# Kernel tuning notes

Hardware: AMD Instinct MI355X
Metric: run time of the kernel (lower is better)

Reference implementation:

```python
import jax, jax.numpy as jnp
import numpy as np

D = 1024
H = 16
HD = D // H
B = 2
S = 2048


def setup_inputs() -> dict:
    key = jax.random.key(0)
    ks = jax.random.split(key, 9)
    sc = 1.0 / np.sqrt(D)
    return {
        "x": jax.random.normal(ks[0], (B, S, D), dtype=jnp.float32),
        "attention_mask": jnp.ones((B, S), dtype=jnp.int32),
        "Wq": jax.random.normal(ks[1], (D, D), dtype=jnp.float32) * sc,
        "bq": jax.random.normal(ks[2], (D,), dtype=jnp.float32) * 0.02,
        "Wk": jax.random.normal(ks[3], (D, D), dtype=jnp.float32) * sc,
        "bk": jax.random.normal(ks[4], (D,), dtype=jnp.float32) * 0.02,
        "Wv": jax.random.normal(ks[5], (D, D), dtype=jnp.float32) * sc,
        "bv": jax.random.normal(ks[6], (D,), dtype=jnp.float32) * 0.02,
        "Wo": jax.random.normal(ks[7], (D, D), dtype=jnp.float32) * sc,
        "bo": jax.random.normal(ks[8], (D,), dtype=jnp.float32) * 0.02,
    }


def reference(x, attention_mask, Wq, bq, Wk, bk, Wv, bv, Wo, bo):
    Bb, Ss, d = x.shape
    # projections (torch Linear: x @ W.T + b; here W stored as [in,out])
    q = (x @ Wq + bq).reshape(Bb, Ss, H, HD).transpose(0, 2, 1, 3)  # [B,H,S,hd]
    k = (x @ Wk + bk).reshape(Bb, Ss, H, HD).transpose(0, 2, 1, 3)
    v = (x @ Wv + bv).reshape(Bb, Ss, H, HD).transpose(0, 2, 1, 3)
    dots = jnp.einsum("bhqd,bhkd->bhqk", q, k) / np.sqrt(HD)  # [B,H,S,S]
    causal = jnp.triu(jnp.ones((Ss, Ss), dtype=bool), k=1)  # True above diagonal
    dots = jnp.where(causal[None, None], -jnp.inf, dots)
    pad = (attention_mask == 0)[:, None, None, :]  # [B,1,1,S]
    dots = jnp.where(pad, -jnp.inf, dots)
    scores = jax.nn.softmax(dots, axis=-1)
    o = jnp.einsum("bhqk,bhkd->bhqd", scores, v)  # [B,H,S,hd]
    o = o.transpose(0, 2, 1, 3).reshape(Bb, Ss, d)
    return o @ Wo + bo
```

## Files before the change

### kernel.cpp

```cpp
#include <hip/hip_runtime.h>

#define D_  1024
#define H_  16
#define HD_ 64
#define B_  2
#define S_  2048
#define M_  (B_*S_)

typedef _Float16 f16;
typedef _Float16 f16x8 __attribute__((ext_vector_type(8)));
typedef _Float16 f16x4 __attribute__((ext_vector_type(4)));
typedef _Float16 f16x2 __attribute__((ext_vector_type(2)));
typedef __fp16   h16x2 __attribute__((ext_vector_type(2)));
typedef float    f32x4 __attribute__((ext_vector_type(4)));

#define GLOAD_LDS16(g, l) \
  __builtin_amdgcn_global_load_lds((__attribute__((address_space(1))) const void*)(g), \
                                   (__attribute__((address_space(3))) void*)(l), 16, 0, 0)

__global__ void k_cvt_x(const float* __restrict__ x, f16* __restrict__ xb) {
  int i = blockIdx.x * blockDim.x + threadIdx.x;
  float4 v = ((const float4*)x)[i];
  f16x4 o = { (f16)v.x, (f16)v.y, (f16)v.z, (f16)v.w };
  ((f16x4*)xb)[i] = o;
}

__global__ void k_twt4(const float* __restrict__ Wq, const float* __restrict__ Wk,
                       const float* __restrict__ Wv, const float* __restrict__ Wo,
                       f16* __restrict__ WT) {
  __shared__ float t[32][33];
  int z = blockIdx.z;
  const float* W = (z == 0) ? Wq : (z == 1) ? Wk : (z == 2) ? Wv : Wo;
  f16* out = WT + (size_t)z * D_ * D_;
  int n0 = blockIdx.x * 32, k0 = blockIdx.y * 32;
  int tx = threadIdx.x, ty = threadIdx.y;
  #pragma unroll
  for (int i = 0; i < 4; i++)
    t[ty + i*8][tx] = W[(size_t)(k0 + ty + i*8) * D_ + n0 + tx];
  __syncthreads();
  #pragma unroll
  for (int i = 0; i < 4; i++)
    out[(size_t)(n0 + ty + i*8) * D_ + k0 + tx] = (f16)t[tx][ty + i*8];
}

template<int MODE>
__device__ __forceinline__ void gemm_body(const f16* __restrict__ A,
                                          const f16* __restrict__ Bt,
                                          const float* __restrict__ bias,
                                          void* __restrict__ Cout) {
  __shared__ __align__(16) f16 lA[2][128 * 32];
  __shared__ __align__(16) f16 lB[2][128 * 32];
  const int tid = threadIdx.x;
  const int wv = tid >> 6, lane = tid & 63;
  const int m0 = blockIdx.y * 128, n0 = blockIdx.x * 128;
  const int fr = lane & 15, fg = lane >> 4;
  const int wm = wv >> 1, wn = wv & 1;
  const int srow = (lane >> 2), skk = (lane & 3) * 8;
  f32x4 acc[4][4] = {};

#define G_STAGE(k0_, c_) do { \
    _Pragma("unroll") \
    for (int it_ = 0; it_ < 2; ++it_) { \
      int ch_ = wv + it_ * 4; \
      int row_ = ch_ * 16 + srow; \
      GLOAD_LDS16(A  + (size_t)(m0 + row_) * D_ + (k0_) + skk, &lA[c_][ch_ * 512]); \
      GLOAD_LDS16(Bt + (size_t)(n0 + row_) * D_ + (k0_) + skk, &lB[c_][ch_ * 512]); \
    } \
  } while (0)

  G_STAGE(0, 0);
  __syncthreads();

  int c = 0;
  for (int k0 = 0; k0 < D_; k0 += 32) {
    if (k0 + 32 < D_) G_STAGE(k0 + 32, c ^ 1);
    f16x8 a[4], b[4];
    #pragma unroll
    for (int i = 0; i < 4; i++) a[i] = *(const f16x8*)&lA[c][(wm*64 + i*16 + fr) * 32 + fg * 8];
    #pragma unroll
    for (int j = 0; j < 4; j++) b[j] = *(const f16x8*)&lB[c][(wn*64 + j*16 + fr) * 32 + fg * 8];
    #pragma unroll
    for (int i = 0; i < 4; i++)
      #pragma unroll
      for (int j = 0; j < 4; j++)
        acc[i][j] = __builtin_amdgcn_mfma_f32_16x16x32_f16(a[i], b[j], acc[i][j], 0, 0, 0);
    __syncthreads();
    c ^= 1;
  }
#undef G_STAGE

  #pragma unroll
  for (int i = 0; i < 4; i++) {
    #pragma unroll
    for (int j = 0; j < 4; j++) {
      int grow0 = m0 + wm*64 + i*16 + fg*4;
      int gcol  = n0 + wn*64 + j*16 + fr;
      float bb = bias[gcol & (D_ - 1)];
      #pragma unroll
      for (int r = 0; r < 4; r++) {
        float val = acc[i][j][r] + bb;
        int grow = grow0 + r;
        if (MODE == 0) {
          int z = gcol >> 10, gl = gcol & (D_ - 1);
          int b = grow >> 11, s = grow & (S_ - 1);
          int h = gl >> 6,  hd = gl & (HD_ - 1);
          ((f16*)Cout)[(size_t)z * (M_ * D_) +
                       ((size_t)(b * H_ + h) * S_ + s) * HD_ + hd] = (f16)val;
        } else {
          ((float*)Cout)[(size_t)grow * D_ + gcol] = val;
        }
      }
    }
  }
}

__global__ __launch_bounds__(256) void k_gemm_qkv(const f16* __restrict__ A,
                                                  const f16* __restrict__ WT0,
                                                  const float* __restrict__ bq,
                                                  const float* __restrict__ bk,
                                                  const float* __restrict__ bv,
                                                  f16* __restrict__ qkv) {
  const int n0 = blockIdx.x * 128;
  const float* bias = (n0 < 1024) ? bq : (n0 < 2048) ? bk : bv;
  gemm_body<0>(A, WT0, bias, qkv);
}

__global__ __launch_bounds__(256) void k_gemm_out(const f16* __restrict__ A,
                                                  const f16* __restrict__ Bt,
                                                  const float* __restrict__ bias,
                                                  float* __restrict__ Cout) {
  gemm_body<1>(A, Bt, bias, Cout);
}

#define POFF 8.65617025f

__global__ __launch_bounds__(256) void k_attn(const f16* __restrict__ Qh,
                                              const f16* __restrict__ Kh,
                                              const f16* __restrict__ Vh,
                                              const int* __restrict__ am,
                                              f16* __restrict__ OpA, f16* __restrict__ OpB,
                                              float* __restrict__ lpA, float* __restrict__ lpB) {
  __shared__ __align__(16) f16 kt[2][64 * 64];
  __shared__ __align__(16) f16 vt[2][64 * 64];
  __shared__ __align__(16) f16 pl[4][32 * 64];

  const int tid = threadIdx.x;
  const int wv = tid >> 6, lane = tid & 63;
  const int fr = lane & 15, fg = lane >> 4;

  const int d = blockIdx.x;
  const int bh = d & 31;
  const int m  = (d >> 5) & 7;
  const int typeB = d >> 8;
  const int b = bh >> 4;

  f16*   Op = typeB ? OpB : OpA;
  float* lp = typeB ? lpB : lpA;

  const f16* Qb = Qh + (size_t)bh * S_ * HD_;
  const f16* Kb = Kh + (size_t)bh * S_ * HD_;
  const f16* Vb = Vh + (size_t)bh * S_ * HD_;
  const int* amb = am + b * S_;
  f16* plw = pl[wv];

  volatile int* flag = (volatile int*)&pl[0][0];
  if (tid == 0) *flag = 1;
  __syncthreads();
  {
    int mv = 1;
    #pragma unroll
    for (int i = 0; i < 8; ++i) mv &= amb[tid * 8 + i];
    if (!mv) *flag = 0;
  }
  __syncthreads();
  const bool allv = (*flag != 0);

  const f16 qs = (f16)0.18033688f;
  const int ksrc = 8 * ((lane & 7) ^ (lane >> 3));
  const int swz = (fr & 7) << 3;
  const int vkk = (tid >> 3) * 2, vd0 = (tid & 7) * 8;
  const int vswz2 = (tid & 3) << 4;
  const f32x4 cinit = { -POFF, -POFF, -POFF, -POFF };
  const f16 one_ = (f16)1.0f;
  const f16x8 onesf = { one_, one_, one_, one_, one_, one_, one_, one_ };

#define STAGE_K(t_, c_) do { \
    const f16* kp_ = Kb + (size_t)((t_) * 64) * HD_; \
    GLOAD_LDS16(kp_ + (size_t)((wv*2+0)*8 + (lane >> 3)) * HD_ + ksrc, &kt[c_][(wv*2+0)*512]); \
    GLOAD_LDS16(kp_ + (size_t)((wv*2+1)*8 + (lane >> 3)) * HD_ + ksrc, &kt[c_][(wv*2+1)*512]); \
  } while (0)

#define LOAD_V(t_) do { \
    const f16* vp_ = Vb + (size_t)((t_) * 64 + vkk) * HD_ + vd0; \
    vA = *(const f16x8*)vp_; vBr = *(const f16x8*)(vp_ + HD_); \
  } while (0)

#define WRITE_V(c_) do { \
    _Pragma("unroll") \
    for (int j_ = 0; j_ < 8; ++j_) { \
      f16x2 pr_ = { vA[j_], vBr[j_] }; \
      *(f16x2*)&vt[c_][(vd0 + j_) * 64 + ((vkk ^ (j_ << 3)) ^ vswz2)] = pr_; \
    } \
  } while (0)

  f16x8 vA, vBr;

  const int qts[2] = { m, 15 - m };
  int s_t0[2], s_t1[2];
  if (!typeB) {
    s_t0[0] = 0;     s_t1[0] = m + 1;
    s_t0[1] = 0;     s_t1[1] = 16 - m;
  } else {
    s_t0[0] = m + 1;  s_t1[0] = 2 * (m + 1);
    s_t0[1] = 16 - m; s_t1[1] = 2 * (16 - m);
  }

  STAGE_K(s_t0[0], 0);
  LOAD_V(s_t0[0]);
  WRITE_V(0);
  __syncthreads();

  int c = 0;
  for (int sg = 0; sg < 2; ++sg) {
    const int qt = qts[sg];
    const int q0w = qt * 128 + wv * 32;

    f16x8 qf[2][2];
    #pragma unroll
    for (int rt = 0; rt < 2; ++rt) {
      f16x8 r0 = *(const f16x8*)&Qb[(size_t)(q0w + rt*16 + fr) * HD_ + fg*8];
      f16x8 r1 = *(const f16x8*)&Qb[(size_t)(q0w + rt*16 + fr) * HD_ + 32 + fg*8];
      qf[rt][0] = r0 * qs; qf[rt][1] = r1 * qs;
    }

    f32x4 accO[2][4] = {};
    f32x4 accL[2] = {};

    for (int t = s_t0[sg]; t < s_t1[sg]; ++t) {
      int nt_ = -1;
      if (t + 1 < s_t1[sg]) nt_ = t + 1;
      else if (sg == 0)     nt_ = s_t0[1];
      if (nt_ >= 0) { STAGE_K(nt_, c ^ 1); LOAD_V(nt_); }

      const int kb = t * 64;
      const int dq = q0w - kb;
      if (dq + 31 >= 0) {
        int tm1 = (dq + 31) >> 4; if (tm1 > 3) tm1 = 3;
        int tm0 = (dq + 15) >> 4; if (tm0 > 3) tm0 = 3;
        const bool fullb = (dq >= 63);

        f32x4 s[2][4];
        #pragma unroll
        for (int rt = 0; rt < 2; ++rt)
          #pragma unroll
          for (int tt = 0; tt < 4; ++tt) s[rt][tt] = cinit;

        __builtin_amdgcn_s_setprio(1);
        #pragma unroll
        for (int tt = 0; tt < 4; ++tt) {
          if (tt <= tm1) {
            const int kr = (tt*16 + fr) * 64;
            f16x8 kf0 = *(const f16x8*)&kt[c][kr + ((     fg*8) ^ swz)];
            f16x8 kf1 = *(const f16x8*)&kt[c][kr + ((32 + fg*8) ^ swz)];
            s[1][tt] = __builtin_amdgcn_mfma_f32_16x16x32_f16(kf0, qf[1][0], s[1][tt], 0, 0, 0);
            s[1][tt] = __builtin_amdgcn_mfma_f32_16x16x32_f16(kf1, qf[1][1], s[1][tt], 0, 0, 0);
            if (tt <= tm0) {
              s[0][tt] = __builtin_amdgcn_mfma_f32_16x16x32_f16(kf0, qf[0][0], s[0][tt], 0, 0, 0);
              s[0][tt] = __builtin_amdgcn_mfma_f32_16x16x32_f16(kf1, qf[0][1], s[0][tt], 0, 0, 0);
            }
          }
        }
        __builtin_amdgcn_s_setprio(0);

        #pragma unroll
        for (int rt = 0; rt < 2; ++rt) {
          const int tmr = rt ? tm1 : tm0;
          if (tmr < 0) continue;
          const int thr = dq + rt*16 + fr;
          #pragma unroll
          for (int tt = 0; tt < 4; ++tt) {
            union { f16x4 v; h16x2 h[2]; } pk;
            pk.v = (f16x4){};
            if (tt <= tmr) {
              float p[4];
              if (allv) {
                #pragma unroll
                for (int r = 0; r < 4; ++r) {
                  float sv = s[rt][tt][r];
                  if (!fullb) sv = (tt*16 + fg*4 + r <= thr) ? sv : -1e30f;
                  p[r] = exp2f(sv);
                }
              } else {
                int4 a4 = *(const int4*)&amb[kb + tt*16 + fg*4];
                #pragma unroll
                for (int r = 0; r < 4; ++r) {
                  float sv = s[rt][tt][r];
                  if (!fullb) sv = (tt*16 + fg*4 + r <= thr) ? sv : -1e30f;
                  float pv = exp2f(sv);
                  int mr_ = (r == 0) ? a4.x : (r == 1) ? a4.y : (r == 2) ? a4.z : a4.w;
                  p[r] = mr_ ? pv : 0.0f;
                }
              }
              pk.h[0] = __builtin_amdgcn_cvt_pkrtz(p[0], p[1]);
              pk.h[1] = __builtin_amdgcn_cvt_pkrtz(p[2], p[3]);
            }
            *(f16x4*)&plw[(rt*16 + fr) * 64 + ((tt*16 + fg*4) ^ swz)] = pk.v;
          }
        }

        __builtin_amdgcn_s_setprio(1);
        #pragma unroll
        for (int ks = 0; ks < 2; ++ks) {
          if (ks <= (tm1 >> 1)) {
            f16x8 vf[4];
            #pragma unroll
            for (int nt = 0; nt < 4; ++nt)
              vf[nt] = *(const f16x8*)&vt[c][(nt*16 + fr) * 64 +
                           ((ks*32 + fg*8) ^ swz ^ (((2*nt + (fr >> 3)) & 3) << 4))];
            #pragma unroll
            for (int rt = 0; rt < 2; ++rt) {
              const int tmr = rt ? tm1 : tm0;
              if (tmr >= 0 && ks <= (tmr >> 1)) {
                f16x8 pa = *(const f16x8*)&plw[(rt*16 + fr) * 64 + ((ks*32 + fg*8) ^ swz)];
                #pragma unroll
                for (int nt = 0; nt < 4; ++nt)
                  accO[rt][nt] = __builtin_amdgcn_mfma_f32_16x16x32_f16(pa, vf[nt], accO[rt][nt], 0, 0, 0);
                accL[rt] = __builtin_amdgcn_mfma_f32_16x16x32_f16(pa, onesf, accL[rt], 0, 0, 0);
              }
            }
          }
        }
        __builtin_amdgcn_s_setprio(0);
      }

      if (nt_ >= 0) WRITE_V(c ^ 1);
      __syncthreads();
      c ^= 1;
    }

    #pragma unroll
    for (int rt = 0; rt < 2; ++rt) {
      if (fr == 0) {
        #pragma unroll
        for (int r = 0; r < 4; ++r)
          lp[(size_t)bh * S_ + q0w + rt*16 + fg*4 + r] = accL[rt][r];
      }
      f16* Oprow = Op + (size_t)bh * (S_ * HD_);
      #pragma unroll
      for (int nt = 0; nt < 4; ++nt) {
        int col = nt*16 + fr;
        #pragma unroll
        for (int r = 0; r < 4; ++r) {
          int row = q0w + rt*16 + fg*4 + r;
          Oprow[(size_t)row * HD_ + col] = (f16)accO[rt][nt][r];
        }
      }
    }
  }

#undef STAGE_K
#undef LOAD_V
#undef WRITE_V
}

__global__ __launch_bounds__(256) void k_comb(const f16* __restrict__ OA,
                                              const f16* __restrict__ OB,
                                              const float* __restrict__ lA,
                                              const float* __restrict__ lB,
                                              f16* __restrict__ Obf) {
  int gid = blockIdx.x * 256 + threadIdx.x;
  int seg = gid & 7, rowg = gid >> 3;
  int bh = rowg >> 11, row = rowg & 2047;
  f16x8 a  = ((const f16x8*)OA)[gid];
  f16x8 b2 = ((const f16x8*)OB)[gid];
  float inv = __builtin_amdgcn_rcpf(lA[rowg] + lB[rowg]);
  f16x8 o;
  #pragma unroll
  for (int j = 0; j < 8; ++j) o[j] = (f16)(((float)a[j] + (float)b2[j]) * inv);
  int bb = bh >> 4, hh = bh & 15;
  *(f16x8*)&Obf[((size_t)(bb * S_ + row)) * D_ + hh * 64 + seg * 8] = o;
}

extern "C" void kernel_launch(void* const* d_in, const int* in_sizes, int n_in,
                              void* d_out, int out_size, void* d_ws, size_t ws_size,
                              hipStream_t stream) {
  const float* x  = (const float*)d_in[0];
  const int*   am = (const int*)d_in[1];
  const float* Wq = (const float*)d_in[2];
  const float* bq = (const float*)d_in[3];
  const float* Wk = (const float*)d_in[4];
  const float* bk = (const float*)d_in[5];
  const float* Wv = (const float*)d_in[6];
  const float* bv = (const float*)d_in[7];
  const float* Wo = (const float*)d_in[8];
  const float* bo = (const float*)d_in[9];

  char* ws = (char*)d_ws;
  f16*   xb  = (f16*)(ws);
  f16*   wt  = (f16*)(ws + (8u  << 20));
  f16*   qkv = (f16*)(ws + (16u << 20));
  f16*   OpA = (f16*)(ws + (40u << 20));
  f16*   OpB = xb;
  float* lpA = (float*)(ws + (8u << 20));
  float* lpB = (float*)(ws + (8u << 20) + (256u << 10));
  f16*   Obf = qkv;

  k_cvt_x<<<4096, 256, 0, stream>>>(x, xb);

  dim3 tb(32, 8), tg4(32, 32, 4);
  k_twt4<<<tg4, tb, 0, stream>>>(Wq, Wk, Wv, Wo, wt);

  k_gemm_qkv<<<dim3(24, 32), 256, 0, stream>>>(xb, wt, bq, bk, bv, qkv);

  k_attn<<<dim3(512), 256, 0, stream>>>(qkv,
                                        qkv + (size_t)M_ * D_,
                                        qkv + 2 * (size_t)M_ * D_,
                                        am, OpA, OpB, lpA, lpB);

  k_comb<<<dim3(2048), 256, 0, stream>>>(OpA, OpB, lpA, lpB, Obf);

  k_gemm_out<<<dim3(8, 32), 256, 0, stream>>>(Obf, wt + 3 * (size_t)(D_ * D_), bo,
                                              (float*)d_out);
}
```

Baseline: 126.0 us.

## Triple-buffer K tiles and flatten attention loop into a two-ahead prefetch pipeline

Flattens the two query-tile segments into a single loop over all K/V tiles. K now uses a triple LDS buffer with async global-to-LDS staging issued two tiles ahead, and V register loads are likewise issued one iteration earlier. The block-wide sync is replaced by a barrier that waits only on older vector-memory ops (vmcnt(4)), so the next prefetch stays in flight across the barrier. This aims to hide global load latency behind MFMA work, at the cost of extra LDS, more register pressure, and hand-tuned waitcnt correctness risk.

```diff
diff --git a/kernel.cpp b/kernel.cpp
--- a/kernel.cpp
+++ b/kernel.cpp
@@ -134,13 +134,20 @@
 
 #define POFF 8.65617025f
 
+#define PIPE_BARRIER() do { \
+    asm volatile("s_waitcnt vmcnt(4) lgkmcnt(0)" ::: "memory"); \
+    __builtin_amdgcn_s_barrier(); \
+    asm volatile("" ::: "memory"); \
+    __builtin_amdgcn_sched_barrier(0); \
+  } while (0)
+
 __global__ __launch_bounds__(256) void k_attn(const f16* __restrict__ Qh,
                                               const f16* __restrict__ Kh,
                                               const f16* __restrict__ Vh,
                                               const int* __restrict__ am,
                                               f16* __restrict__ OpA, f16* __restrict__ OpB,
                                               float* __restrict__ lpA, float* __restrict__ lpB) {
-  __shared__ __align__(16) f16 kt[2][64 * 64];
+  __shared__ __align__(16) f16 kt[3][64 * 64];
   __shared__ __align__(16) f16 vt[2][64 * 64];
   __shared__ __align__(16) f16 pl[4][32 * 64];
 
@@ -206,144 +213,39 @@
   f16x8 vA, vBr;
 
   const int qts[2] = { m, 15 - m };
-  int s_t0[2], s_t1[2];
-  if (!typeB) {
-    s_t0[0] = 0;     s_t1[0] = m + 1;
-    s_t0[1] = 0;     s_t1[1] = 16 - m;
-  } else {
-    s_t0[0] = m + 1;  s_t1[0] = 2 * (m + 1);
-    s_t0[1] = 16 - m; s_t1[1] = 2 * (16 - m);
+  int t00, t01, t10, t11;
+  if (!typeB) { t00 = 0;      t01 = m + 1;        t10 = 0;      t11 = 16 - m; }
+  else        { t00 = m + 1;  t01 = 2 * (m + 1);  t10 = 16 - m; t11 = 2 * (16 - m); }
+  const int n0 = t01 - t00;
+  const int ntot = n0 + (t11 - t10);
+  #define TILE_OF(g_) (((g_) < n0) ? (t00 + (g_)) : (t10 + (g_) - n0))
+
+  LOAD_V(TILE_OF(0));
+  STAGE_K(TILE_OF(0), 0);
+  WRITE_V(0);
+  LOAD_V(TILE_OF(1));
+  STAGE_K(TILE_OF(1), 1);
+  PIPE_BARRIER();
+
+  int sg = 0;
+  int q0w = qts[0] * 128 + wv * 32;
+  f16x8 qf[2][2];
+  #pragma unroll
+  for (int rt = 0; rt < 2; ++rt) {
+    f16x8 r0 = *(const f16x8*)&Qb[(size_t)(q0w + rt*16 + fr) * HD_ + fg*8];
+    f16x8 r1 = *(const f16x8*)&Qb[(size_t)(q0w + rt*16 + fr) * HD_ + 32 + fg*8];
+    qf[rt][0] = r0 * qs; qf[rt][1] = r1 * qs;
   }
-
-  STAGE_K(s_t0[0], 0);
-  LOAD_V(s_t0[0]);
-  WRITE_V(0);
-  __syncthreads();
-
-  int c = 0;
-  for (int sg = 0; sg < 2; ++sg) {
-    const int qt = qts[sg];
-    const int q0w = qt * 128 + wv * 32;
-
-    f16x8 qf[2][2];
-    #pragma unroll
-    for (int rt = 0; rt < 2; ++rt) {
-      f16x8 r0 = *(const f16x8*)&Qb[(size_t)(q0w + rt*16 + fr) * HD_ + fg*8];
-      f16x8 r1 = *(const f16x8*)&Qb[(size_t)(q0w + rt*16 + fr) * HD_ + 32 + fg*8];
-      qf[rt][0] = r0 * qs; qf[rt][1] = r1 * qs;
-    }
-
-    f32x4 accO[2][4] = {};
-    f32x4 accL[2] = {};
-
-    for (int t = s_t0[sg]; t < s_t1[sg]; ++t) {
-      int nt_ = -1;
-      if (t + 1 < s_t1[sg]) nt_ = t + 1;
-      else if (sg == 0)     nt_ = s_t0[1];
-      if (nt_ >= 0) { STAGE_K(nt_, c ^ 1); LOAD_V(nt_); }
-
-      const int kb = t * 64;
-      const int dq = q0w - kb;
-      if (dq + 31 >= 0) {
-        int tm1 = (dq + 31) >> 4; if (tm1 > 3) tm1 = 3;
-        int tm0 = (dq + 15) >> 4; if (tm0 > 3) tm0 = 3;
-        const bool fullb = (dq >= 63);
-
-        f32x4 s[2][4];
-        #pragma unroll
-        for (int rt = 0; rt < 2; ++rt)
-          #pragma unroll
-          for (int tt = 0; tt < 4; ++tt) s[rt][tt] = cinit;
-
-        __builtin_amdgcn_s_setprio(1);
-        #pragma unroll
-        for (int tt = 0; tt < 4; ++tt) {
-          if (tt <= tm1) {
-            const int kr = (tt*16 + fr) * 64;
-            f16x8 kf0 = *(const f16x8*)&kt[c][kr + ((     fg*8) ^ swz)];
-            f16x8 kf1 = *(const f16x8*)&kt[c][kr + ((32 + fg*8) ^ swz)];
-            s[1][tt] = __builtin_amdgcn_mfma_f32_16x16x32_f16(kf0, qf[1][0], s[1][tt], 0, 0, 0);
-            s[1][tt] = __builtin_amdgcn_mfma_f32_16x16x32_f16(kf1, qf[1][1], s[1][tt], 0, 0, 0);
-            if (tt <= tm0) {
-              s[0][tt] = __builtin_amdgcn_mfma_f32_16x16x32_f16(kf0, qf[0][0], s[0][tt], 0, 0, 0);
-              s[0][tt] = __builtin_amdgcn_mfma_f32_16x16x32_f16(kf1, qf[0][1], s[0][tt], 0, 0, 0);
-            }
-          }
-        }
-        __builtin_amdgcn_s_setprio(0);
-
-        #pragma unroll
-        for (int rt = 0; rt < 2; ++rt) {
-          const int tmr = rt ? tm1 : tm0;
-          if (tmr < 0) continue;
-          const int thr = dq + rt*16 + fr;
-          #pragma unroll
-          for (int tt = 0; tt < 4; ++tt) {
-            union { f16x4 v; h16x2 h[2]; } pk;
-            pk.v = (f16x4){};
-            if (tt <= tmr) {
-              float p[4];
-              if (allv) {
-                #pragma unroll
-                for (int r = 0; r < 4; ++r) {
-                  float sv = s[rt][tt][r];
-                  if (!fullb) sv = (tt*16 + fg*4 + r <= thr) ? sv : -1e30f;
-                  p[r] = exp2f(sv);
-                }
-              } else {
-                int4 a4 = *(const int4*)&amb[kb + tt*16 + fg*4];
-                #pragma unroll
-                for (int r = 0; r < 4; ++r) {
-                  float sv = s[rt][tt][r];
-                  if (!fullb) sv = (tt*16 + fg*4 + r <= thr) ? sv : -1e30f;
-                  float pv = exp2f(sv);
-                  int mr_ = (r == 0) ? a4.x : (r == 1) ? a4.y : (r == 2) ? a4.z : a4.w;
-                  p[r] = mr_ ? pv : 0.0f;
-                }
-              }
-              pk.h[0] = __builtin_amdgcn_cvt_pkrtz(p[0], p[1]);
-              pk.h[1] = __builtin_amdgcn_cvt_pkrtz(p[2], p[3]);
-            }
-            *(f16x4*)&plw[(rt*16 + fr) * 64 + ((tt*16 + fg*4) ^ swz)] = pk.v;
-          }
-        }
-
-        __builtin_amdgcn_s_setprio(1);
-        #pragma unroll
-        for (int ks = 0; ks < 2; ++ks) {
-          if (ks <= (tm1 >> 1)) {
-            f16x8 vf[4];
-            #pragma unroll
-            for (int nt = 0; nt < 4; ++nt)
-              vf[nt] = *(const f16x8*)&vt[c][(nt*16 + fr) * 64 +
-                           ((ks*32 + fg*8) ^ swz ^ (((2*nt + (fr >> 3)) & 3) << 4))];
-            #pragma unroll
-            for (int rt = 0; rt < 2; ++rt) {
-              const int tmr = rt ? tm1 : tm0;
-              if (tmr >= 0 && ks <= (tmr >> 1)) {
-                f16x8 pa = *(const f16x8*)&plw[(rt*16 + fr) * 64 + ((ks*32 + fg*8) ^ swz)];
-                #pragma unroll
-                for (int nt = 0; nt < 4; ++nt)
-                  accO[rt][nt] = __builtin_amdgcn_mfma_f32_16x16x32_f16(pa, vf[nt], accO[rt][nt], 0, 0, 0);
-                accL[rt] = __builtin_amdgcn_mfma_f32_16x16x32_f16(pa, onesf, accL[rt], 0, 0, 0);
-              }
-            }
-          }
-        }
-        __builtin_amdgcn_s_setprio(0);
-      }
-
-      if (nt_ >= 0) WRITE_V(c ^ 1);
-      __syncthreads();
-      c ^= 1;
-    }
-
+  f32x4 accO[2][4] = {};
+  f32x4 accL[2] = {};
+
+  auto do_epi = [&](int q0w_) {
     #pragma unroll
     for (int rt = 0; rt < 2; ++rt) {
       if (fr == 0) {
         #pragma unroll
         for (int r = 0; r < 4; ++r)
-          lp[(size_t)bh * S_ + q0w + rt*16 + fg*4 + r] = accL[rt][r];
+          lp[(size_t)bh * S_ + q0w_ + rt*16 + fg*4 + r] = accL[rt][r];
       }
       f16* Oprow = Op + (size_t)bh * (S_ * HD_);
       #pragma unroll
@@ -351,13 +253,136 @@
         int col = nt*16 + fr;
         #pragma unroll
         for (int r = 0; r < 4; ++r) {
-          int row = q0w + rt*16 + fg*4 + r;
+          int row = q0w_ + rt*16 + fg*4 + r;
           Oprow[(size_t)row * HD_ + col] = (f16)accO[rt][nt][r];
         }
       }
     }
+  };
+
+  for (int g = 0; g < ntot; ++g) {
+    if (g == n0) {
+      do_epi(q0w);
+      sg = 1;
+      q0w = qts[1] * 128 + wv * 32;
+      #pragma unroll
+      for (int rt = 0; rt < 2; ++rt) {
+        f16x8 r0 = *(const f16x8*)&Qb[(size_t)(q0w + rt*16 + fr) * HD_ + fg*8];
+        f16x8 r1 = *(const f16x8*)&Qb[(size_t)(q0w + rt*16 + fr) * HD_ + 32 + fg*8];
+        qf[rt][0] = r0 * qs; qf[rt][1] = r1 * qs;
+        accL[rt] = (f32x4){};
+        #pragma unroll
+        for (int nt = 0; nt < 4; ++nt) accO[rt][nt] = (f32x4){};
+      }
+    }
+
+    const int t = TILE_OF(g);
+    const int cK = g % 3, cV = g & 1;
+
+    if (g + 1 < ntot) WRITE_V((g + 1) & 1);
+    if (g + 2 < ntot) {
+      const int tp = TILE_OF(g + 2);
+      LOAD_V(tp);
+      STAGE_K(tp, (g + 2) % 3);
+    }
+
+    const int kb = t * 64;
+    const int dq = q0w - kb;
+    if (dq + 31 >= 0) {
+      int tm1 = (dq + 31) >> 4; if (tm1 > 3) tm1 = 3;
+      int tm0 = (dq + 15) >> 4; if (tm0 > 3) tm0 = 3;
+      const bool fullb = (dq >= 63);
+
+      f32x4 s[2][4];
+      #pragma unroll
+      for (int rt = 0; rt < 2; ++rt)
+        #pragma unroll
+        for (int tt = 0; tt < 4; ++tt) s[rt][tt] = cinit;
+
+      __builtin_amdgcn_s_setprio(1);
+      #pragma unroll
+      for (int tt = 0; tt < 4; ++tt) {
+        if (tt <= tm1) {
+          const int kr = (tt*16 + fr) * 64;
+          f16x8 kf0 = *(const f16x8*)&kt[cK][kr + ((     fg*8) ^ swz)];
+          f16x8 kf1 = *(const f16x8*)&kt[cK][kr + ((32 + fg*8) ^ swz)];
+          s[1][tt] = __builtin_amdgcn_mfma_f32_16x16x32_f16(kf0, qf[1][0], s[1][tt], 0, 0, 0);
+          s[1][tt] = __builtin_amdgcn_mfma_f32_16x16x32_f16(kf1, qf[1][1], s[1][tt], 0, 0, 0);
+          if (tt <= tm0) {
+            s[0][tt] = __builtin_amdgcn_mfma_f32_16x16x32_f16(kf0, qf[0][0], s[0][tt], 0, 0, 0);
+            s[0][tt] = __builtin_amdgcn_mfma_f32_16x16x32_f16(kf1, qf[0][1], s[0][tt], 0, 0, 0);
+          }
+        }
+      }
+      __builtin_amdgcn_s_setprio(0);
+
+      #pragma unroll
+      for (int rt = 0; rt < 2; ++rt) {
+        const int tmr = rt ? tm1 : tm0;
+        if (tmr < 0) continue;
+        const int thr = dq + rt*16 + fr;
+        #pragma unroll
+        for (int tt = 0; tt < 4; ++tt) {
+          union { f16x4 v; h16x2 h[2]; } pk;
+          pk.v = (f16x4){};
+          if (tt <= tmr) {
+            float p[4];
+            if (allv) {
+              #pragma unroll
+              for (int r = 0; r < 4; ++r) {
+                float sv = s[rt][tt][r];
+                if (!fullb) sv = (tt*16 + fg*4 + r <= thr) ? sv : -1e30f;
+                p[r] = exp2f(sv);
+              }
+            } else {
+              int4 a4 = *(const int4*)&amb[kb + tt*16 + fg*4];
+              #pragma unroll
+              for (int r = 0; r < 4; ++r) {
+                float sv = s[rt][tt][r];
+                if (!fullb) sv = (tt*16 + fg*4 + r <= thr) ? sv : -1e30f;
+                float pv = exp2f(sv);
+                int mr_ = (r == 0) ? a4.x : (r == 1) ? a4.y : (r == 2) ? a4.z : a4.w;
+                p[r] = mr_ ? pv : 0.0f;
+              }
+            }
+            pk.h[0] = __builtin_amdgcn_cvt_pkrtz(p[0], p[1]);
+            pk.h[1] = __builtin_amdgcn_cvt_pkrtz(p[2], p[3]);
+          }
+          *(f16x4*)&plw[(rt*16 + fr) * 64 + ((tt*16 + fg*4) ^ swz)] = pk.v;
+        }
+      }
+
+      __builtin_amdgcn_s_setprio(1);
+      #pragma unroll
+      for (int ks = 0; ks < 2; ++ks) {
+        if (ks <= (tm1 >> 1)) {
+          f16x8 vf[4];
+          #pragma unroll
+          for (int nt = 0; nt < 4; ++nt)
+            vf[nt] = *(const f16x8*)&vt[cV][(nt*16 + fr) * 64 +
+                         ((ks*32 + fg*8) ^ swz ^ (((2*nt + (fr >> 3)) & 3) << 4))];
+          #pragma unroll
+          for (int rt = 0; rt < 2; ++rt) {
+            const int tmr = rt ? tm1 : tm0;
+            if (tmr >= 0 && ks <= (tmr >> 1)) {
+              f16x8 pa = *(const f16x8*)&plw[(rt*16 + fr) * 64 + ((ks*32 + fg*8) ^ swz)];
+              #pragma unroll
+              for (int nt = 0; nt < 4; ++nt)
+                accO[rt][nt] = __builtin_amdgcn_mfma_f32_16x16x32_f16(pa, vf[nt], accO[rt][nt], 0, 0, 0);
+              accL[rt] = __builtin_amdgcn_mfma_f32_16x16x32_f16(pa, onesf, accL[rt], 0, 0, 0);
+            }
+          }
+        }
+      }
+      __builtin_amdgcn_s_setprio(0);
+    }
+
+    PIPE_BARRIER();
   }
 
+  do_epi(q0w);
+
+#undef TILE_OF
 #undef STAGE_K
 #undef LOAD_V
 #undef WRITE_V
```

Result: no change. 128.4 us (+2.0%).

## Fuse split-attention combine into output GEMM and merge prep kernels

Applied to the files above, without the earlier changes.

The separate combine kernel that merged the two partial attention outputs and normalized them is removed. The output projection GEMM now loads both partial outputs per tile, combines and scales them by precomputed reciprocal row sums held in LDS, and writes the f16 result into shared memory. The x conversion and weight transpose kernels are merged into one launch. This removes two launches and a full round trip of the combined tensor through global memory, at the cost of register-path A loads with ALU work inside the GEMM loop instead of direct global-to-LDS copies, and the combine is redone by each of the 8 column blocks.

```diff
diff --git a/kernel.cpp b/kernel.cpp
--- a/kernel.cpp
+++ b/kernel.cpp
@@ -18,41 +18,46 @@
   __builtin_amdgcn_global_load_lds((__attribute__((address_space(1))) const void*)(g), \
                                    (__attribute__((address_space(3))) void*)(l), 16, 0, 0)
 
-__global__ void k_cvt_x(const float* __restrict__ x, f16* __restrict__ xb) {
-  int i = blockIdx.x * blockDim.x + threadIdx.x;
-  float4 v = ((const float4*)x)[i];
-  f16x4 o = { (f16)v.x, (f16)v.y, (f16)v.z, (f16)v.w };
-  ((f16x4*)xb)[i] = o;
-}
-
-__global__ void k_twt4(const float* __restrict__ Wq, const float* __restrict__ Wk,
+__global__ void k_prep(const float* __restrict__ x, f16* __restrict__ xb,
+                       const float* __restrict__ Wq, const float* __restrict__ Wk,
                        const float* __restrict__ Wv, const float* __restrict__ Wo,
                        f16* __restrict__ WT) {
   __shared__ float t[32][33];
-  int z = blockIdx.z;
-  const float* W = (z == 0) ? Wq : (z == 1) ? Wk : (z == 2) ? Wv : Wo;
-  f16* out = WT + (size_t)z * D_ * D_;
-  int n0 = blockIdx.x * 32, k0 = blockIdx.y * 32;
-  int tx = threadIdx.x, ty = threadIdx.y;
-  #pragma unroll
-  for (int i = 0; i < 4; i++)
-    t[ty + i*8][tx] = W[(size_t)(k0 + ty + i*8) * D_ + n0 + tx];
-  __syncthreads();
-  #pragma unroll
-  for (int i = 0; i < 4; i++)
-    out[(size_t)(n0 + ty + i*8) * D_ + k0 + tx] = (f16)t[tx][ty + i*8];
+  const int bid = blockIdx.x, tid = threadIdx.x;
+  if (bid < 4096) {
+    int i = bid * 256 + tid;
+    float4 v = ((const float4*)x)[i];
+    f16x4 o = { (f16)v.x, (f16)v.y, (f16)v.z, (f16)v.w };
+    ((f16x4*)xb)[i] = o;
+  } else {
+    int r = bid - 4096;
+    const int z = r >> 10; r &= 1023;
+    const int n0 = (r & 31) * 32, k0 = (r >> 5) * 32;
+    const float* W = (z == 0) ? Wq : (z == 1) ? Wk : (z == 2) ? Wv : Wo;
+    f16* out = WT + (size_t)z * D_ * D_;
+    const int tx = tid & 31, ty = tid >> 5;
+    #pragma unroll
+    for (int i = 0; i < 4; i++)
+      t[ty + i*8][tx] = W[(size_t)(k0 + ty + i*8) * D_ + n0 + tx];
+    __syncthreads();
+    #pragma unroll
+    for (int i = 0; i < 4; i++)
+      out[(size_t)(n0 + ty + i*8) * D_ + k0 + tx] = (f16)t[tx][ty + i*8];
+  }
 }
 
-template<int MODE>
-__device__ __forceinline__ void gemm_body(const f16* __restrict__ A,
-                                          const f16* __restrict__ Bt,
-                                          const float* __restrict__ bias,
-                                          void* __restrict__ Cout) {
+__global__ __launch_bounds__(256) void k_gemm_qkv(const f16* __restrict__ A,
+                                                  const f16* __restrict__ Bt,
+                                                  const float* __restrict__ bq,
+                                                  const float* __restrict__ bk,
+                                                  const float* __restrict__ bv,
+                                                  f16* __restrict__ qkv) {
   __shared__ __align__(16) f16 lA[2][128 * 32];
   __shared__ __align__(16) f16 lB[2][128 * 32];
   const int tid = threadIdx.x;
   const int wv = tid >> 6, lane = tid & 63;
   const int m0 = blockIdx.y * 128, n0 = blockIdx.x * 128;
+  const float* bias = (n0 < 1024) ? bq : (n0 < 2048) ? bk : bv;
   const int fr = lane & 15, fg = lane >> 4;
   const int wm = wv >> 1, wn = wv & 1;
   const int srow = (lane >> 2), skk = (lane & 3) * 8;
@@ -100,36 +105,121 @@
       for (int r = 0; r < 4; r++) {
         float val = acc[i][j][r] + bb;
         int grow = grow0 + r;
-        if (MODE == 0) {
-          int z = gcol >> 10, gl = gcol & (D_ - 1);
-          int b = grow >> 11, s = grow & (S_ - 1);
-          int h = gl >> 6,  hd = gl & (HD_ - 1);
-          ((f16*)Cout)[(size_t)z * (M_ * D_) +
-                       ((size_t)(b * H_ + h) * S_ + s) * HD_ + hd] = (f16)val;
-        } else {
-          ((float*)Cout)[(size_t)grow * D_ + gcol] = val;
-        }
+        int z = gcol >> 10, gl = gcol & (D_ - 1);
+        int b = grow >> 11, s = grow & (S_ - 1);
+        int h = gl >> 6,  hd = gl & (HD_ - 1);
+        qkv[(size_t)z * (M_ * D_) + ((size_t)(b * H_ + h) * S_ + s) * HD_ + hd] = (f16)val;
       }
     }
   }
 }
 
-__global__ __launch_bounds__(256) void k_gemm_qkv(const f16* __restrict__ A,
-                                                  const f16* __restrict__ WT0,
-                                                  const float* __restrict__ bq,
-                                                  const float* __restrict__ bk,
-                                                  const float* __restrict__ bv,
-                                                  f16* __restrict__ qkv) {
-  const int n0 = blockIdx.x * 128;
-  const float* bias = (n0 < 1024) ? bq : (n0 < 2048) ? bk : bv;
-  gemm_body<0>(A, WT0, bias, qkv);
-}
-
-__global__ __launch_bounds__(256) void k_gemm_out(const f16* __restrict__ A,
-                                                  const f16* __restrict__ Bt,
-                                                  const float* __restrict__ bias,
-                                                  float* __restrict__ Cout) {
-  gemm_body<1>(A, Bt, bias, Cout);
+__global__ __launch_bounds__(256) void k_gemm_out2(const f16* __restrict__ OA,
+                                                   const f16* __restrict__ OB,
+                                                   const float* __restrict__ la,
+                                                   const float* __restrict__ lb,
+                                                   const f16* __restrict__ Bt,
+                                                   const float* __restrict__ bias,
+                                                   float* __restrict__ Cout) {
+  __shared__ __align__(16) f16 sA[2][128 * 32];
+  __shared__ __align__(16) f16 sB[2][128 * 32];
+  __shared__ float linv[16 * 128];
+  const int tid = threadIdx.x;
+  const int wv = tid >> 6, lane = tid & 63;
+  const int m0 = blockIdx.y * 128, n0 = blockIdx.x * 128;
+  const int fr = lane & 15, fg = lane >> 4;
+  const int wm = wv >> 1, wn = wv & 1;
+  const int srow = (lane >> 2), skk = (lane & 3) * 8;
+  f32x4 acc[4][4] = {};
+
+  for (int i = tid; i < 2048; i += 256) {
+    int hh = i >> 7, row = i & 127;
+    int grow = m0 + row;
+    size_t rowg = (size_t)((grow >> 11) * 16 + hh) * S_ + (grow & (S_ - 1));
+    linv[i] = __builtin_amdgcn_rcpf(la[rowg] + lb[rowg]);
+  }
+
+  f16x8 rA[2], rB[2];
+
+#define A_LOAD(k0_) do { \
+    const int hh_ = (k0_) >> 6; \
+    _Pragma("unroll") \
+    for (int it_ = 0; it_ < 2; ++it_) { \
+      int row_ = (wv + it_*4) * 16 + srow; \
+      int grow_ = m0 + row_; \
+      size_t off_ = ((size_t)((grow_ >> 11) * 16 + hh_) * S_ + (grow_ & (S_ - 1))) * HD_ \
+                    + (((k0_) + skk) & (HD_ - 1)); \
+      rA[it_] = *(const f16x8*)&OA[off_]; \
+      rB[it_] = *(const f16x8*)&OB[off_]; \
+    } \
+  } while (0)
+
+#define A_WRITE(k0_, c_) do { \
+    const int hh_ = (k0_) >> 6; \
+    _Pragma("unroll") \
+    for (int it_ = 0; it_ < 2; ++it_) { \
+      int ch_ = wv + it_*4; \
+      float inv_ = linv[hh_ * 128 + ch_*16 + srow]; \
+      union { f16x8 v; h16x2 h[4]; } o_; \
+      _Pragma("unroll") \
+      for (int j_ = 0; j_ < 4; ++j_) { \
+        float e0_ = ((float)rA[it_][2*j_]   + (float)rB[it_][2*j_])   * inv_; \
+        float e1_ = ((float)rA[it_][2*j_+1] + (float)rB[it_][2*j_+1]) * inv_; \
+        o_.h[j_] = __builtin_amdgcn_cvt_pkrtz(e0_, e1_); \
+      } \
+      *(f16x8*)&sA[c_][ch_*512 + lane*8] = o_.v; \
+    } \
+  } while (0)
+
+#define B_STAGE(k0_, c_) do { \
+    _Pragma("unroll") \
+    for (int it_ = 0; it_ < 2; ++it_) { \
+      int ch_ = wv + it_*4; \
+      int row_ = ch_*16 + srow; \
+      GLOAD_LDS16(Bt + (size_t)(n0 + row_) * D_ + (k0_) + skk, &sB[c_][ch_*512]); \
+    } \
+  } while (0)
+
+  A_LOAD(0);
+  B_STAGE(0, 0);
+  __syncthreads();
+  A_WRITE(0, 0);
+  __syncthreads();
+
+  int c = 0;
+  for (int k0 = 0; k0 < D_; k0 += 32) {
+    const bool pre = (k0 + 32 < D_);
+    if (pre) { A_LOAD(k0 + 32); B_STAGE(k0 + 32, c ^ 1); }
+    f16x8 a[4], b[4];
+    #pragma unroll
+    for (int i = 0; i < 4; i++) a[i] = *(const f16x8*)&sA[c][(wm*64 + i*16 + fr) * 32 + fg * 8];
+    #pragma unroll
+    for (int j = 0; j < 4; j++) b[j] = *(const f16x8*)&sB[c][(wn*64 + j*16 + fr) * 32 + fg * 8];
+    #pragma unroll
+    for (int i = 0; i < 4; i++)
+      #pragma unroll
+      for (int j = 0; j < 4; j++)
+        acc[i][j] = __builtin_amdgcn_mfma_f32_16x16x32_f16(a[i], b[j], acc[i][j], 0, 0, 0);
+    if (pre) A_WRITE(k0 + 32, c ^ 1);
+    __syncthreads();
+    c ^= 1;
+  }
+
+  #pragma unroll
+  for (int i = 0; i < 4; i++) {
+    #pragma unroll
+    for (int j = 0; j < 4; j++) {
+      int grow0 = m0 + wm*64 + i*16 + fg*4;
+      int gcol  = n0 + wn*64 + j*16 + fr;
+      float bb = bias[gcol];
+      #pragma unroll
+      for (int r = 0; r < 4; r++)
+        Cout[(size_t)(grow0 + r) * D_ + gcol] = acc[i][j][r] + bb;
+    }
+  }
+#undef A_LOAD
+#undef A_WRITE
+#undef B_STAGE
 }
 
 #define POFF 8.65617025f
@@ -363,24 +453,6 @@
 #undef WRITE_V
 }
 
-__global__ __launch_bounds__(256) void k_comb(const f16* __restrict__ OA,
-                                              const f16* __restrict__ OB,
-                                              const float* __restrict__ lA,
-                                              const float* __restrict__ lB,
-                                              f16* __restrict__ Obf) {
-  int gid = blockIdx.x * 256 + threadIdx.x;
-  int seg = gid & 7, rowg = gid >> 3;
-  int bh = rowg >> 11, row = rowg & 2047;
-  f16x8 a  = ((const f16x8*)OA)[gid];
-  f16x8 b2 = ((const f16x8*)OB)[gid];
-  float inv = __builtin_amdgcn_rcpf(lA[rowg] + lB[rowg]);
-  f16x8 o;
-  #pragma unroll
-  for (int j = 0; j < 8; ++j) o[j] = (f16)(((float)a[j] + (float)b2[j]) * inv);
-  int bb = bh >> 4, hh = bh & 15;
-  *(f16x8*)&Obf[((size_t)(bb * S_ + row)) * D_ + hh * 64 + seg * 8] = o;
-}
-
 extern "C" void kernel_launch(void* const* d_in, const int* in_sizes, int n_in,
                               void* d_out, int out_size, void* d_ws, size_t ws_size,
                               hipStream_t stream) {
@@ -403,12 +475,8 @@
   f16*   OpB = xb;
   float* lpA = (float*)(ws + (8u << 20));
   float* lpB = (float*)(ws + (8u << 20) + (256u << 10));
-  f16*   Obf = qkv;
-
-  k_cvt_x<<<4096, 256, 0, stream>>>(x, xb);
-
-  dim3 tb(32, 8), tg4(32, 32, 4);
-  k_twt4<<<tg4, tb, 0, stream>>>(Wq, Wk, Wv, Wo, wt);
+
+  k_prep<<<8192, 256, 0, stream>>>(x, xb, Wq, Wk, Wv, Wo, wt);
 
   k_gemm_qkv<<<dim3(24, 32), 256, 0, stream>>>(xb, wt, bq, bk, bv, qkv);
 
@@ -417,8 +485,7 @@
                                         qkv + 2 * (size_t)M_ * D_,
                                         am, OpA, OpB, lpA, lpB);
 
-  k_comb<<<dim3(2048), 256, 0, stream>>>(OpA, OpB, lpA, lpB, Obf);
-
-  k_gemm_out<<<dim3(8, 32), 256, 0, stream>>>(Obf, wt + 3 * (size_t)(D_ * D_), bo,
-                                              (float*)d_out);
+  k_gemm_out2<<<dim3(8, 32), 256, 0, stream>>>(OpA, OpB, lpA, lpB,
+                                               wt + 3 * (size_t)(D_ * D_), bo,
+                                               (float*)d_out);
 }
```

Result: slower. 139.6 us (+10.8%).
